# Performance work log

Hardware: AMD Instinct MI355X
Metric: run time of the kernel (lower is better)

## Reference

```python
import jax, jax.numpy as jnp
import numpy as np

NHEADS = 8
HEAD_DIM = 64  # odim // nheads = 512 // 8


def setup_inputs() -> dict:
    key = jax.random.key(0)
    ks = jax.random.split(key, 5)
    B, S, D = 2, 4096, 512
    scale = 1.0 / np.sqrt(D)
    return {
        "m_feats": jax.random.normal(ks[0], (B, S, D), dtype=jnp.float32),
        "Wc": jax.random.normal(ks[1], (2 * D, D), dtype=jnp.float32) * scale,
        "bc": jax.random.normal(ks[2], (2 * D,), dtype=jnp.float32) * 0.01,
        "Wv": jax.random.normal(ks[3], (D, D), dtype=jnp.float32) * scale,
        "bv": jax.random.normal(ks[4], (D,), dtype=jnp.float32) * 0.01,
    }


def reference(m_feats, Wc, bc, Wv, bv):
    # eval mode: dropout(p=0.5) is identity
    B, S, D = m_feats.shape
    H, Dh = NHEADS, HEAD_DIM
    m_k = m_feats @ Wv.T + bv                    # [B,S,D]
    m_trans = m_feats @ Wc.T + bc                # [B,S,2D]
    m_q, m_v = m_trans[..., :D], m_trans[..., D:]
    # torch.split into contiguous per-head chunks == reshape to [B,S,H,Dh]
    k = m_k.reshape(B, S, H, Dh)
    q = m_q.reshape(B, S, H, Dh)
    v = m_v.reshape(B, S, H, Dh)
    # scores[b,h,i,j] = k_i . q_j / sqrt(Dh); softmax over j (the q axis)
    scores = jnp.einsum("bihd,bjhd->bhij", k, q) / np.sqrt(Dh).astype(np.float32)
    w = jax.nn.softmax(scores, axis=-1)          # [B,H,S,S]
    r = jnp.einsum("bhij,bjhd->bihd", w, v).reshape(B, S, D)
    return m_feats + r
```

## Files before the change

kernel.cpp:

```cpp
#include <hip/hip_runtime.h>

#define MTOT 8192

typedef __attribute__((ext_vector_type(8))) short bf16x8;
typedef __attribute__((ext_vector_type(4))) float f32x4;

#if __has_builtin(__builtin_amdgcn_exp2f)
#define EXP2F __builtin_amdgcn_exp2f
#else
#define EXP2F exp2f
#endif

#define SC 0.18033688011112042f
#define LDP 72
#define CTS 136

static __device__ __forceinline__ unsigned short tb(float f) {
  union { float f; unsigned int i; } x;
  x.f = f;
  return (unsigned short)(x.i >> 16);
}
static __device__ __forceinline__ unsigned int pkt(float a, float b) {
  union { float f; unsigned int i; } xa, xb;
  xa.f = a; xb.f = b;
  return (xa.i >> 16) | (xb.i & 0xFFFF0000u);
}
static __device__ __forceinline__ bf16x8 ld8f32_bf16(const float* __restrict__ p) {
  f32x4 lo = *(const f32x4*)p;
  f32x4 hi = *(const f32x4*)(p + 4);
  union { unsigned int u[4]; bf16x8 v; } r;
  r.u[0] = pkt(lo[0], lo[1]);
  r.u[1] = pkt(lo[2], lo[3]);
  r.u[2] = pkt(hi[0], hi[1]);
  r.u[3] = pkt(hi[2], hi[3]);
  return r.v;
}

static __device__ __forceinline__ void stage16(const unsigned short* g,
                                               unsigned short* l, int lane) {
#if __has_builtin(__builtin_amdgcn_global_load_lds)
  __builtin_amdgcn_global_load_lds(
      (const __attribute__((address_space(1))) void*)g,
      (__attribute__((address_space(3))) void*)l, 16, 0, 0);
#else
  *(uint4*)(l + lane * 8) = *(const uint4*)g;
#endif
}

__global__ __launch_bounds__(256) void convert_bf16(
    const float* __restrict__ mf,
    const float* __restrict__ Wc,
    const float* __restrict__ Wv,
    unsigned short* __restrict__ dst)
{
  const size_t NA = (size_t)MTOT * 512;
  const size_t NW = (size_t)1536 * 512;
  const size_t total = (NA + NW) / 8;
  for (size_t u = (size_t)blockIdx.x * blockDim.x + threadIdx.x; u < total;
       u += (size_t)gridDim.x * blockDim.x) {
    const size_t el = u * 8;
    const float* src;
    if (el < NA) {
      src = mf + el;
    } else {
      const size_t e2 = el - NA;
      src = (e2 < (size_t)1024 * 512) ? (Wc + e2) : (Wv + (e2 - (size_t)1024 * 512));
    }
    f32x4 lo = *(const f32x4*)src;
    f32x4 hi = *(const f32x4*)(src + 4);
    uint4 pk;
    pk.x = pkt(lo[0], lo[1]); pk.y = pkt(lo[2], lo[3]);
    pk.z = pkt(hi[0], hi[1]); pk.w = pkt(hi[2], hi[3]);
    *(uint4*)(dst + el) = pk;
  }
}

__global__ __launch_bounds__(256) void gemm_fast(
    const unsigned short* __restrict__ Abf,
    const unsigned short* __restrict__ Wbf,
    const float* __restrict__ bc,
    const float* __restrict__ bv,
    unsigned short* __restrict__ ws)
{
  const int cpx = (int)gridDim.x >> 3;
  const int bid = ((int)blockIdx.x & 7) * cpx + ((int)blockIdx.x >> 3);
  const int tn = bid % 12, tm = bid / 12;
  const int w = threadIdx.x >> 6, lane = threadIdx.x & 63;
  const int n = lane & 15, q = lane >> 4;

  __shared__ alignas(16) unsigned short smem[2 * 128 * LDP];
  unsigned short* As = smem;
  unsigned short* Bs = smem + 128 * 64;

  f32x4 acc[4][4] = {};
  const int rowA0 = tm * 128, colB0 = tn * 128;
  const int lr = lane >> 3;
  const int lc = (lane & 7) * 8;
  const unsigned short* gA = Abf + (size_t)(rowA0 + w * 32 + lr) * 512 + lc;
  const unsigned short* gB = Wbf + (size_t)(colB0 + w * 32 + lr) * 512 + lc;

  for (int kc = 0; kc < 512; kc += 64) {
#pragma unroll
    for (int rr = 0; rr < 4; ++rr) {
      stage16(gA + (size_t)rr * 8 * 512 + kc, As + (w * 32 + rr * 8) * 64, lane);
      stage16(gB + (size_t)rr * 8 * 512 + kc, Bs + (w * 32 + rr * 8) * 64, lane);
    }
    __syncthreads();
#pragma unroll
    for (int ks = 0; ks < 2; ++ks) {
      bf16x8 a[4], b[4];
#pragma unroll
      for (int si = 0; si < 4; ++si)
        a[si] = *(const bf16x8*)(&As[((w >> 1) * 64 + si * 16 + n) * 64 + ks * 32 + q * 8]);
#pragma unroll
      for (int sj = 0; sj < 4; ++sj)
        b[sj] = *(const bf16x8*)(&Bs[((w & 1) * 64 + sj * 16 + n) * 64 + ks * 32 + q * 8]);
#pragma unroll
      for (int si = 0; si < 4; ++si)
#pragma unroll
        for (int sj = 0; sj < 4; ++sj)
          acc[si][sj] = __builtin_amdgcn_mfma_f32_16x16x32_bf16(a[si], b[sj], acc[si][sj], 0, 0, 0);
    }
    __syncthreads();
  }

  unsigned short* Ct = smem;
  const bool isV = (tn >= 4 && tn < 8);
  const int rl0 = (w >> 1) * 64, cl0 = (w & 1) * 64;

  if (!isV) {
    const bool isK = (tn >= 8);
#pragma unroll
    for (int sj = 0; sj < 4; ++sj) {
      const int c = colB0 + sj * 16 + n;
      const float bias = isK ? bv[c - 1024] : bc[c];
#pragma unroll
      for (int si = 0; si < 4; ++si)
#pragma unroll
        for (int r = 0; r < 4; ++r) {
          float v = acc[si][sj][r] + bias;
          if (isK) v *= SC;
          Ct[(rl0 + si * 16 + q * 4 + r) * CTS + cl0 + sj * 16 + n] = tb(v);
        }
    }
  } else {
#pragma unroll
    for (int sj = 0; sj < 4; ++sj) {
      const float bias = bc[colB0 + sj * 16 + n];
#pragma unroll
      for (int si = 0; si < 4; ++si) {
        uint2 pk;
        pk.x = pkt(acc[si][sj][0] + bias, acc[si][sj][1] + bias);
        pk.y = pkt(acc[si][sj][2] + bias, acc[si][sj][3] + bias);
        *(uint2*)(&Ct[(cl0 + sj * 16 + n) * CTS + rl0 + si * 16 + q * 4]) = pk;
      }
    }
  }
  __syncthreads();

  const int rk = threadIdx.x & 7, rr2 = threadIdx.x >> 3;
#pragma unroll
  for (int rp = 0; rp < 4; ++rp) {
    const int row = rp * 32 + rr2;
#pragma unroll
    for (int ch = 0; ch < 2; ++ch) {
      const int col = ch * 64 + rk * 8;
      bf16x8 v = *(const bf16x8*)(&Ct[row * CTS + col]);
      if (!isV) {
        const int srow = rowA0 + row;
        const int bb = srow >> 12, ss = srow & 4095;
        const int cg = colB0 + col;
        const int cl = (cg >= 1024) ? (cg - 1024) : cg;
        const int hh = cl >> 6, dh0 = cl & 63;
        unsigned short* base = (cg >= 1024) ? (ws + (size_t)2 * MTOT * 512) : ws;
        *(bf16x8*)(base + ((size_t)((bb * 8 + hh) * 4096 + ss)) * 64 + dh0) = v;
      } else {
        const int cv = (tn - 4) * 128 + row;
        const int hh = cv >> 6, dh0 = cv & 63;
        const int sg = rowA0 + col;
        const int bb = sg >> 12, ss = sg & 4095;
        *(bf16x8*)(ws + (size_t)MTOT * 512 +
                   ((size_t)((bb * 8 + hh) * 64 + dh0)) * 4096 + ss) = v;
      }
    }
  }
}

__global__ __launch_bounds__(256) void gemm_qvk(
    const float* __restrict__ mf,
    const float* __restrict__ Wc,
    const float* __restrict__ bc,
    const float* __restrict__ Wv,
    const float* __restrict__ bv,
    unsigned short* __restrict__ ws,
    int nct)
{
  const int cpx = (int)gridDim.x >> 3;
  const int bid = ((int)blockIdx.x & 7) * cpx + ((int)blockIdx.x >> 3);
  const int tn = bid % nct, tm = bid / nct;
  const int w = threadIdx.x >> 6, lane = threadIdx.x & 63;
  const int n = lane & 15, q = lane >> 4;

  __shared__ alignas(16) unsigned short smem[2 * 128 * LDP];
  unsigned short* As = smem;
  unsigned short* Bs = smem + 128 * LDP;

  f32x4 acc[4][4] = {};
  const int rowA0 = tm * 128, colB0 = tn * 128;
  const int sr = threadIdx.x >> 4;
  const int sc = (threadIdx.x & 15) * 4;

  for (int kc = 0; kc < 512; kc += 64) {
    __syncthreads();
#pragma unroll
    for (int rr = 0; rr < 8; ++rr) {
      const int row = rr * 16 + sr;
      f32x4 av = *(const f32x4*)(mf + (size_t)(rowA0 + row) * 512 + kc + sc);
      uint2 ap; ap.x = pkt(av[0], av[1]); ap.y = pkt(av[2], av[3]);
      *(uint2*)(&As[row * LDP + sc]) = ap;
      const int c = colB0 + row;
      const float* bsrc = (c < 1024) ? (Wc + (size_t)c * 512)
                                     : (Wv + (size_t)(c - 1024) * 512);
      f32x4 bvx = *(const f32x4*)(bsrc + kc + sc);
      uint2 bp; bp.x = pkt(bvx[0], bvx[1]); bp.y = pkt(bvx[2], bvx[3]);
      *(uint2*)(&Bs[row * LDP + sc]) = bp;
    }
    __syncthreads();
#pragma unroll
    for (int ks = 0; ks < 2; ++ks) {
      bf16x8 a[4], b[4];
#pragma unroll
      for (int si = 0; si < 4; ++si)
        a[si] = *(const bf16x8*)(&As[((w >> 1) * 64 + si * 16 + n) * LDP + ks * 32 + q * 8]);
#pragma unroll
      for (int sj = 0; sj < 4; ++sj)
        b[sj] = *(const bf16x8*)(&Bs[((w & 1) * 64 + sj * 16 + n) * LDP + ks * 32 + q * 8]);
#pragma unroll
      for (int si = 0; si < 4; ++si)
#pragma unroll
        for (int sj = 0; sj < 4; ++sj)
          acc[si][sj] = __builtin_amdgcn_mfma_f32_16x16x32_bf16(a[si], b[sj], acc[si][sj], 0, 0, 0);
    }
  }

  __syncthreads();
  unsigned short* Ct = smem;
  const bool isV = (tn >= 4 && tn < 8);
  const int rl0 = (w >> 1) * 64, cl0 = (w & 1) * 64;

  if (!isV) {
    const bool isK = (tn >= 8);
#pragma unroll
    for (int sj = 0; sj < 4; ++sj) {
      const int c = colB0 + sj * 16 + n;
      const float bias = isK ? bv[c - 1024] : bc[c];
#pragma unroll
      for (int si = 0; si < 4; ++si)
#pragma unroll
        for (int r = 0; r < 4; ++r) {
          float v = acc[si][sj][r] + bias;
          if (isK) v *= SC;
          Ct[(rl0 + si * 16 + q * 4 + r) * CTS + cl0 + sj * 16 + n] = tb(v);
        }
    }
  } else {
#pragma unroll
    for (int sj = 0; sj < 4; ++sj) {
      const float bias = bc[colB0 + sj * 16 + n];
#pragma unroll
      for (int si = 0; si < 4; ++si) {
        uint2 pk;
        pk.x = pkt(acc[si][sj][0] + bias, acc[si][sj][1] + bias);
        pk.y = pkt(acc[si][sj][2] + bias, acc[si][sj][3] + bias);
        *(uint2*)(&Ct[(cl0 + sj * 16 + n) * CTS + rl0 + si * 16 + q * 4]) = pk;
      }
    }
  }
  __syncthreads();

  const int rk = threadIdx.x & 7, rr2 = threadIdx.x >> 3;
#pragma unroll
  for (int rp = 0; rp < 4; ++rp) {
    const int row = rp * 32 + rr2;
#pragma unroll
    for (int ch = 0; ch < 2; ++ch) {
      const int col = ch * 64 + rk * 8;
      bf16x8 v = *(const bf16x8*)(&Ct[row * CTS + col]);
      if (!isV) {
        const int srow = rowA0 + row;
        const int bb = srow >> 12, ss = srow & 4095;
        const int cg = colB0 + col;
        const int cl = (cg >= 1024) ? (cg - 1024) : cg;
        const int hh = cl >> 6, dh0 = cl & 63;
        unsigned short* base = (cg >= 1024) ? (ws + (size_t)2 * MTOT * 512) : ws;
        *(bf16x8*)(base + ((size_t)((bb * 8 + hh) * 4096 + ss)) * 64 + dh0) = v;
      } else {
        const int cv = (tn - 4) * 128 + row;
        const int hh = cv >> 6, dh0 = cv & 63;
        const int sg = rowA0 + col;
        const int bb = sg >> 12, ss = sg & 4095;
        *(bf16x8*)(ws + (size_t)MTOT * 512 +
                   ((size_t)((bb * 8 + hh) * 64 + dh0)) * 4096 + ss) = v;
      }
    }
  }
}

template <bool KWS>
__global__ __launch_bounds__(128, 2) void attn_kernel(
    const unsigned short* __restrict__ qvws,
    const float* __restrict__ mf,
    const float* __restrict__ Wv,
    const float* __restrict__ bv,
    float* __restrict__ out)
{
  const int bid = blockIdx.x;
  const int bh = ((bid & 7) << 1) | ((bid >> 3) & 1);
  const int ib = bid >> 4;
  const int b_ = bh >> 3, h = bh & 7;
  const int w = threadIdx.x >> 6, lane = threadIdx.x & 63;
  const int n = lane & 15, q = lane >> 4;
  const int i0 = ib * 64;

  __shared__ alignas(16) unsigned short PK[2][64 * LDP];
  __shared__ float lbuf[2][64];

  const unsigned short* Qb = qvws + (size_t)(bh * 4096) * 64;
  const unsigned short* Vb = qvws + (size_t)MTOT * 512 + (size_t)(bh * 64) * 4096;

  bf16x8 aK[4][2];
  if (KWS) {
    const unsigned short* Kb = qvws + (size_t)2 * MTOT * 512 + (size_t)(bh * 4096) * 64;
#pragma unroll
    for (int sub = 0; sub < 4; ++sub)
#pragma unroll
      for (int s = 0; s < 2; ++s)
        aK[sub][s] = *(const bf16x8*)(Kb + (size_t)(i0 + sub * 16 + n) * 64 + s * 32 + q * 8);
  } else {
    f32x4 ka[2][4] = {};
    for (int kk = 0; kk < 512; kk += 32) {
      bf16x8 a0 = ld8f32_bf16(mf + (size_t)(b_ * 4096 + i0 + (2 * w + 0) * 16 + n) * 512 + kk + q * 8);
      bf16x8 a1 = ld8f32_bf16(mf + (size_t)(b_ * 4096 + i0 + (2 * w + 1) * 16 + n) * 512 + kk + q * 8);
#pragma unroll
      for (int t = 0; t < 4; ++t) {
        bf16x8 bw = ld8f32_bf16(Wv + (size_t)(h * 64 + t * 16 + n) * 512 + kk + q * 8);
        ka[0][t] = __builtin_amdgcn_mfma_f32_16x16x32_bf16(a0, bw, ka[0][t], 0, 0, 0);
        ka[1][t] = __builtin_amdgcn_mfma_f32_16x16x32_bf16(a1, bw, ka[1][t], 0, 0, 0);
      }
    }
#pragma unroll
    for (int sl = 0; sl < 2; ++sl)
#pragma unroll
      for (int t = 0; t < 4; ++t) {
        const float bias = bv[h * 64 + t * 16 + n];
#pragma unroll
        for (int r = 0; r < 4; ++r)
          PK[0][((2 * w + sl) * 16 + q * 4 + r) * LDP + t * 16 + n] =
              tb((ka[sl][t][r] + bias) * SC);
      }
    __syncthreads();
#pragma unroll
    for (int sub = 0; sub < 4; ++sub)
#pragma unroll
      for (int s = 0; s < 2; ++s)
        aK[sub][s] = *(const bf16x8*)(&PK[0][(sub * 16 + n) * LDP + s * 32 + q * 8]);
    __syncthreads();
  }

  f32x4 o[4][4] = {};
  float lsc[4] = {0.0f, 0.0f, 0.0f, 0.0f};
  unsigned short* Pw = &PK[w][0];
  const int jbase = w * 2048;

  bf16x8 bq[4][2], bvv[4][2];
#pragma unroll
  for (int jt = 0; jt < 4; ++jt)
#pragma unroll
    for (int s = 0; s < 2; ++s)
      bq[jt][s] = *(const bf16x8*)(Qb + (size_t)(jbase + jt * 16 + n) * 64 + s * 32 + q * 8);
#pragma unroll
  for (int t = 0; t < 4; ++t)
#pragma unroll
    for (int s = 0; s < 2; ++s)
      bvv[t][s] = *(const bf16x8*)(Vb + (size_t)(t * 16 + n) * 4096 + jbase + s * 32 + q * 8);

  for (int it = 0; it < 32; ++it) {
    const int j1 = jbase + ((it + 1) & 31) * 64;

    f32x4 c[2][4];
#pragma unroll
    for (int jt = 0; jt < 4; ++jt) {
      f32x4 z = {};
      z = __builtin_amdgcn_mfma_f32_16x16x32_bf16(bq[jt][0], aK[0][0], z, 0, 0, 0);
      z = __builtin_amdgcn_mfma_f32_16x16x32_bf16(bq[jt][1], aK[0][1], z, 0, 0, 0);
      c[0][jt] = z;
    }

#pragma unroll
    for (int sub = 0; sub < 4; ++sub) {
      const int cur = sub & 1, nxt = cur ^ 1;
      if (sub < 3) {
#pragma unroll
        for (int jt = 0; jt < 4; ++jt) {
          f32x4 z = {};
          z = __builtin_amdgcn_mfma_f32_16x16x32_bf16(bq[jt][0], aK[sub + 1][0], z, 0, 0, 0);
          z = __builtin_amdgcn_mfma_f32_16x16x32_bf16(bq[jt][1], aK[sub + 1][1], z, 0, 0, 0);
          c[nxt][jt] = z;
        }
      }
      if (sub == 2) {
#pragma unroll
        for (int jt = 0; jt < 4; ++jt)
#pragma unroll
          for (int s = 0; s < 2; ++s)
            bq[jt][s] = *(const bf16x8*)(Qb + (size_t)(j1 + jt * 16 + n) * 64 + s * 32 + q * 8);
      }

#pragma unroll
      for (int jt = 0; jt < 4; ++jt) {
        float e0 = EXP2F(c[cur][jt][0]), e1 = EXP2F(c[cur][jt][1]);
        float e2 = EXP2F(c[cur][jt][2]), e3 = EXP2F(c[cur][jt][3]);
        lsc[sub] += (e0 + e1) + (e2 + e3);
        uint2 pk;
        pk.x = pkt(e0, e1);
        pk.y = pkt(e2, e3);
        *(uint2*)(Pw + (sub * 16 + n) * LDP + jt * 16 + q * 4) = pk;
      }

      asm volatile("s_waitcnt lgkmcnt(0)" ::: "memory");

#pragma unroll
      for (int s = 0; s < 2; ++s) {
        bf16x8 pa = *(const bf16x8*)(Pw + (sub * 16 + n) * LDP + s * 32 + q * 8);
#pragma unroll
        for (int t = 0; t < 4; ++t)
          o[sub][t] = __builtin_amdgcn_mfma_f32_16x16x32_bf16(pa, bvv[t][s], o[sub][t], 0, 0, 0);
      }
    }

#pragma unroll
    for (int t = 0; t < 4; ++t)
#pragma unroll
      for (int s = 0; s < 2; ++s)
        bvv[t][s] = *(const bf16x8*)(Vb + (size_t)(t * 16 + n) * 4096 + j1 + s * 32 + q * 8);
  }

  float lw[4];
#pragma unroll
  for (int sub = 0; sub < 4; ++sub) {
    float v = lsc[sub];
    v += __shfl_xor(v, 16, 64);
    v += __shfl_xor(v, 32, 64);
    lw[sub] = v;
  }

  __syncthreads();
  float* mO = (float*)&PK[0][0];
  const int ebase = (w == 0) ? 0 : 32;
  const int rbase = (w == 0) ? 32 : 0;
  const int esub0 = (w == 0) ? 2 : 0;
  const int ksub0 = (w == 0) ? 0 : 2;
#pragma unroll
  for (int sl = 0; sl < 2; ++sl) {
    const int sub = esub0 + sl;
#pragma unroll
    for (int t = 0; t < 4; ++t)
#pragma unroll
      for (int r = 0; r < 4; ++r)
        mO[(ebase + sl * 16 + q * 4 + r) * 68 + t * 16 + n] = o[sub][t][r];
  }
  if (lane < 16) {
#pragma unroll
    for (int sub = 0; sub < 4; ++sub)
      lbuf[w][sub * 16 + lane] = lw[sub];
  }
  __syncthreads();
#pragma unroll
  for (int sl = 0; sl < 2; ++sl) {
    const int sub = ksub0 + sl;
    float li[4];
#pragma unroll
    for (int r = 0; r < 4; ++r) {
      const int il = sub * 16 + q * 4 + r;
      li[r] = 1.0f / (lbuf[0][il] + lbuf[1][il]);
    }
#pragma unroll
    for (int t = 0; t < 4; ++t) {
#pragma unroll
      for (int r = 0; r < 4; ++r) {
        const int i = i0 + sub * 16 + q * 4 + r;
        const int dh = t * 16 + n;
        const size_t idx = (size_t)(b_ * 4096 + i) * 512 + h * 64 + dh;
        out[idx] = (o[sub][t][r] + mO[(rbase + sl * 16 + q * 4 + r) * 68 + t * 16 + n]) * li[r]
                   + mf[idx];
      }
    }
  }
}

extern "C" void kernel_launch(void* const* d_in, const int* in_sizes, int n_in,
                              void* d_out, int out_size, void* d_ws, size_t ws_size,
                              hipStream_t stream) {
  const float* mf = (const float*)d_in[0];
  const float* Wc = (const float*)d_in[1];
  const float* bc = (const float*)d_in[2];
  const float* Wv = (const float*)d_in[3];
  const float* bv = (const float*)d_in[4];
  float* out = (float*)d_out;
  unsigned short* ws = (unsigned short*)d_ws;

  const size_t elQ = (size_t)MTOT * 512;
  const bool kws = ws_size >= (size_t)3 * elQ * 2;

  if (kws) {
    unsigned short* Abf = (unsigned short*)out;
    unsigned short* Wbf = Abf + (size_t)MTOT * 512;
    convert_bf16<<<2048, 256, 0, stream>>>(mf, Wc, Wv, Abf);
    gemm_fast<<<768, 256, 0, stream>>>(Abf, Wbf, bc, bv, ws);
    attn_kernel<true><<<1024, 128, 0, stream>>>(ws, mf, Wv, bv, out);
  } else {
    gemm_qvk<<<64 * 8, 256, 0, stream>>>(mf, Wc, bc, Wv, bv, ws, 8);
    attn_kernel<false><<<1024, 128, 0, stream>>>(ws, mf, Wv, bv, out);
  }
}
```

Before: 237.1 us.

## Use 128x64 tiles with XOR-swizzled LDS in projection GEMM

The bf16 projection GEMM moves from 128x128 to 128x64 output tiles, which doubles the grid to 1536 blocks and shrinks the shared-memory footprint. LDS staging now uses an XOR swizzle on 16-byte chunks to avoid bank conflicts on unpadded rows. The epilogue is reworked for the narrower tile, using a separate stride for the Q/K staging buffer. The goal is better occupancy and wave balance across CUs and fewer LDS conflicts, at the cost of less A-tile reuse per block.

```diff
diff --git a/kernel.cpp b/kernel.cpp
--- a/kernel.cpp
+++ b/kernel.cpp
@@ -14,6 +14,7 @@
 #define SC 0.18033688011112042f
 #define LDP 72
 #define CTS 136
+#define CTQ 72
 
 static __device__ __forceinline__ unsigned short tb(float f) {
   union { float f; unsigned int i; } x;
@@ -84,26 +85,152 @@
 {
   const int cpx = (int)gridDim.x >> 3;
   const int bid = ((int)blockIdx.x & 7) * cpx + ((int)blockIdx.x >> 3);
-  const int tn = bid % 12, tm = bid / 12;
+  const int tn = bid % 24, tm = bid / 24;
   const int w = threadIdx.x >> 6, lane = threadIdx.x & 63;
   const int n = lane & 15, q = lane >> 4;
 
+  __shared__ alignas(16) unsigned short smem[128 * 64 + 64 * 64];
+  unsigned short* As = smem;
+  unsigned short* Bs = smem + 128 * 64;
+
+  f32x4 acc[4][2] = {};
+  const int rowA0 = tm * 128, colB0 = tn * 64;
+  const int lrow = lane >> 3;
+  const int sw = ((lane & 7) ^ lrow) * 8;
+  const unsigned short* gA = Abf + (size_t)(rowA0 + w * 32 + lrow) * 512 + sw;
+  const unsigned short* gB = Wbf + (size_t)(colB0 + w * 16 + lrow) * 512 + sw;
+
+  for (int kc = 0; kc < 512; kc += 64) {
+#pragma unroll
+    for (int rr = 0; rr < 4; ++rr)
+      stage16(gA + (size_t)rr * 8 * 512 + kc, As + (w * 32 + rr * 8) * 64, lane);
+#pragma unroll
+    for (int rr = 0; rr < 2; ++rr)
+      stage16(gB + (size_t)rr * 8 * 512 + kc, Bs + (w * 16 + rr * 8) * 64, lane);
+    __syncthreads();
+#pragma unroll
+    for (int ks = 0; ks < 2; ++ks) {
+      const int ch = ((ks * 4 + q) ^ (n & 7)) * 8;
+      bf16x8 a[4], b[2];
+#pragma unroll
+      for (int si = 0; si < 4; ++si)
+        a[si] = *(const bf16x8*)(&As[((w >> 1) * 64 + si * 16 + n) * 64 + ch]);
+#pragma unroll
+      for (int sj = 0; sj < 2; ++sj)
+        b[sj] = *(const bf16x8*)(&Bs[((w & 1) * 32 + sj * 16 + n) * 64 + ch]);
+#pragma unroll
+      for (int si = 0; si < 4; ++si)
+#pragma unroll
+        for (int sj = 0; sj < 2; ++sj)
+          acc[si][sj] = __builtin_amdgcn_mfma_f32_16x16x32_bf16(a[si], b[sj], acc[si][sj], 0, 0, 0);
+    }
+    __syncthreads();
+  }
+
+  unsigned short* Ct = smem;
+  const bool isV = (tn >= 8 && tn < 16);
+  const int rl0 = (w >> 1) * 64, cl0 = (w & 1) * 32;
+
+  if (!isV) {
+    const bool isK = (tn >= 16);
+#pragma unroll
+    for (int sj = 0; sj < 2; ++sj) {
+      const int c = colB0 + cl0 + sj * 16 + n;
+      const float bias = isK ? bv[c - 1024] : bc[c];
+#pragma unroll
+      for (int si = 0; si < 4; ++si)
+#pragma unroll
+        for (int r = 0; r < 4; ++r) {
+          float v = acc[si][sj][r] + bias;
+          if (isK) v *= SC;
+          Ct[(rl0 + si * 16 + q * 4 + r) * CTQ + cl0 + sj * 16 + n] = tb(v);
+        }
+    }
+  } else {
+#pragma unroll
+    for (int sj = 0; sj < 2; ++sj) {
+      const float bias = bc[colB0 + cl0 + sj * 16 + n];
+#pragma unroll
+      for (int si = 0; si < 4; ++si) {
+        uint2 pk;
+        pk.x = pkt(acc[si][sj][0] + bias, acc[si][sj][1] + bias);
+        pk.y = pkt(acc[si][sj][2] + bias, acc[si][sj][3] + bias);
+        *(uint2*)(&Ct[(cl0 + sj * 16 + n) * CTS + rl0 + si * 16 + q * 4]) = pk;
+      }
+    }
+  }
+  __syncthreads();
+
+  if (!isV) {
+    const int rk = threadIdx.x & 7, rr2 = threadIdx.x >> 3;
+#pragma unroll
+    for (int rp = 0; rp < 4; ++rp) {
+      const int row = rp * 32 + rr2;
+      const int col = rk * 8;
+      bf16x8 v = *(const bf16x8*)(&Ct[row * CTQ + col]);
+      const int srow = rowA0 + row;
+      const int bb = srow >> 12, ss = srow & 4095;
+      const int cg = colB0 + col;
+      const int cl = (cg >= 1024) ? (cg - 1024) : cg;
+      const int hh = cl >> 6, dh0 = cl & 63;
+      unsigned short* base = (cg >= 1024) ? (ws + (size_t)2 * MTOT * 512) : ws;
+      *(bf16x8*)(base + ((size_t)((bb * 8 + hh) * 4096 + ss)) * 64 + dh0) = v;
+    }
+  } else {
+    const int rk = threadIdx.x & 15, rr2 = threadIdx.x >> 4;
+#pragma unroll
+    for (int rp = 0; rp < 4; ++rp) {
+      const int row = rp * 16 + rr2;
+      const int col = rk * 8;
+      bf16x8 v = *(const bf16x8*)(&Ct[row * CTS + col]);
+      const int cv = (tn - 8) * 64 + row;
+      const int hh = cv >> 6, dh0 = cv & 63;
+      const int sg = rowA0 + col;
+      const int bb = sg >> 12, ss = sg & 4095;
+      *(bf16x8*)(ws + (size_t)MTOT * 512 +
+                 ((size_t)((bb * 8 + hh) * 64 + dh0)) * 4096 + ss) = v;
+    }
+  }
+}
+
+__global__ __launch_bounds__(256) void gemm_qvk(
+    const float* __restrict__ mf,
+    const float* __restrict__ Wc,
+    const float* __restrict__ bc,
+    const float* __restrict__ Wv,
+    const float* __restrict__ bv,
+    unsigned short* __restrict__ ws,
+    int nct)
+{
+  const int cpx = (int)gridDim.x >> 3;
+  const int bid = ((int)blockIdx.x & 7) * cpx + ((int)blockIdx.x >> 3);
+  const int tn = bid % nct, tm = bid / nct;
+  const int w = threadIdx.x >> 6, lane = threadIdx.x & 63;
+  const int n = lane & 15, q = lane >> 4;
+
   __shared__ alignas(16) unsigned short smem[2 * 128 * LDP];
   unsigned short* As = smem;
-  unsigned short* Bs = smem + 128 * 64;
+  unsigned short* Bs = smem + 128 * LDP;
 
   f32x4 acc[4][4] = {};
   const int rowA0 = tm * 128, colB0 = tn * 128;
-  const int lr = lane >> 3;
-  const int lc = (lane & 7) * 8;
-  const unsigned short* gA = Abf + (size_t)(rowA0 + w * 32 + lr) * 512 + lc;
-  const unsigned short* gB = Wbf + (size_t)(colB0 + w * 32 + lr) * 512 + lc;
+  const int sr = threadIdx.x >> 4;
+  const int sc = (threadIdx.x & 15) * 4;
 
   for (int kc = 0; kc < 512; kc += 64) {
-#pragma unroll
-    for (int rr = 0; rr < 4; ++rr) {
-      stage16(gA + (size_t)rr * 8 * 512 + kc, As + (w * 32 + rr * 8) * 64, lane);
-      stage16(gB + (size_t)rr * 8 * 512 + kc, Bs + (w * 32 + rr * 8) * 64, lane);
+    __syncthreads();
+#pragma unroll
+    for (int rr = 0; rr < 8; ++rr) {
+      const int row = rr * 16 + sr;
+      f32x4 av = *(const f32x4*)(mf + (size_t)(rowA0 + row) * 512 + kc + sc);
+      uint2 ap; ap.x = pkt(av[0], av[1]); ap.y = pkt(av[2], av[3]);
+      *(uint2*)(&As[row * LDP + sc]) = ap;
+      const int c = colB0 + row;
+      const float* bsrc = (c < 1024) ? (Wc + (size_t)c * 512)
+                                     : (Wv + (size_t)(c - 1024) * 512);
+      f32x4 bvx = *(const f32x4*)(bsrc + kc + sc);
+      uint2 bp; bp.x = pkt(bvx[0], bvx[1]); bp.y = pkt(bvx[2], bvx[3]);
+      *(uint2*)(&Bs[row * LDP + sc]) = bp;
     }
     __syncthreads();
 #pragma unroll
@@ -111,19 +238,19 @@
       bf16x8 a[4], b[4];
 #pragma unroll
       for (int si = 0; si < 4; ++si)
-        a[si] = *(const bf16x8*)(&As[((w >> 1) * 64 + si * 16 + n) * 64 + ks * 32 + q * 8]);
+        a[si] = *(const bf16x8*)(&As[((w >> 1) * 64 + si * 16 + n) * LDP + ks * 32 + q * 8]);
 #pragma unroll
       for (int sj = 0; sj < 4; ++sj)
-        b[sj] = *(const bf16x8*)(&Bs[((w & 1) * 64 + sj * 16 + n) * 64 + ks * 32 + q * 8]);
+        b[sj] = *(const bf16x8*)(&Bs[((w & 1) * 64 + sj * 16 + n) * LDP + ks * 32 + q * 8]);
 #pragma unroll
       for (int si = 0; si < 4; ++si)
 #pragma unroll
         for (int sj = 0; sj < 4; ++sj)
           acc[si][sj] = __builtin_amdgcn_mfma_f32_16x16x32_bf16(a[si], b[sj], acc[si][sj], 0, 0, 0);
     }
-    __syncthreads();
-  }
-
+  }
+
+  __syncthreads();
   unsigned short* Ct = smem;
   const bool isV = (tn >= 4 && tn < 8);
   const int rl0 = (w >> 1) * 64, cl0 = (w & 1) * 64;
@@ -186,126 +313,6 @@
   }
 }
 
-__global__ __launch_bounds__(256) void gemm_qvk(
-    const float* __restrict__ mf,
-    const float* __restrict__ Wc,
-    const float* __restrict__ bc,
-    const float* __restrict__ Wv,
-    const float* __restrict__ bv,
-    unsigned short* __restrict__ ws,
-    int nct)
-{
-  const int cpx = (int)gridDim.x >> 3;
-  const int bid = ((int)blockIdx.x & 7) * cpx + ((int)blockIdx.x >> 3);
-  const int tn = bid % nct, tm = bid / nct;
-  const int w = threadIdx.x >> 6, lane = threadIdx.x & 63;
-  const int n = lane & 15, q = lane >> 4;
-
-  __shared__ alignas(16) unsigned short smem[2 * 128 * LDP];
-  unsigned short* As = smem;
-  unsigned short* Bs = smem + 128 * LDP;
-
-  f32x4 acc[4][4] = {};
-  const int rowA0 = tm * 128, colB0 = tn * 128;
-  const int sr = threadIdx.x >> 4;
-  const int sc = (threadIdx.x & 15) * 4;
-
-  for (int kc = 0; kc < 512; kc += 64) {
-    __syncthreads();
-#pragma unroll
-    for (int rr = 0; rr < 8; ++rr) {
-      const int row = rr * 16 + sr;
-      f32x4 av = *(const f32x4*)(mf + (size_t)(rowA0 + row) * 512 + kc + sc);
-      uint2 ap; ap.x = pkt(av[0], av[1]); ap.y = pkt(av[2], av[3]);
-      *(uint2*)(&As[row * LDP + sc]) = ap;
-      const int c = colB0 + row;
-      const float* bsrc = (c < 1024) ? (Wc + (size_t)c * 512)
-                                     : (Wv + (size_t)(c - 1024) * 512);
-      f32x4 bvx = *(const f32x4*)(bsrc + kc + sc);
-      uint2 bp; bp.x = pkt(bvx[0], bvx[1]); bp.y = pkt(bvx[2], bvx[3]);
-      *(uint2*)(&Bs[row * LDP + sc]) = bp;
-    }
-    __syncthreads();
-#pragma unroll
-    for (int ks = 0; ks < 2; ++ks) {
-      bf16x8 a[4], b[4];
-#pragma unroll
-      for (int si = 0; si < 4; ++si)
-        a[si] = *(const bf16x8*)(&As[((w >> 1) * 64 + si * 16 + n) * LDP + ks * 32 + q * 8]);
-#pragma unroll
-      for (int sj = 0; sj < 4; ++sj)
-        b[sj] = *(const bf16x8*)(&Bs[((w & 1) * 64 + sj * 16 + n) * LDP + ks * 32 + q * 8]);
-#pragma unroll
-      for (int si = 0; si < 4; ++si)
-#pragma unroll
-        for (int sj = 0; sj < 4; ++sj)
-          acc[si][sj] = __builtin_amdgcn_mfma_f32_16x16x32_bf16(a[si], b[sj], acc[si][sj], 0, 0, 0);
-    }
-  }
-
-  __syncthreads();
-  unsigned short* Ct = smem;
-  const bool isV = (tn >= 4 && tn < 8);
-  const int rl0 = (w >> 1) * 64, cl0 = (w & 1) * 64;
-
-  if (!isV) {
-    const bool isK = (tn >= 8);
-#pragma unroll
-    for (int sj = 0; sj < 4; ++sj) {
-      const int c = colB0 + sj * 16 + n;
-      const float bias = isK ? bv[c - 1024] : bc[c];
-#pragma unroll
-      for (int si = 0; si < 4; ++si)
-#pragma unroll
-        for (int r = 0; r < 4; ++r) {
-          float v = acc[si][sj][r] + bias;
-          if (isK) v *= SC;
-          Ct[(rl0 + si * 16 + q * 4 + r) * CTS + cl0 + sj * 16 + n] = tb(v);
-        }
-    }
-  } else {
-#pragma unroll
-    for (int sj = 0; sj < 4; ++sj) {
-      const float bias = bc[colB0 + sj * 16 + n];
-#pragma unroll
-      for (int si = 0; si < 4; ++si) {
-        uint2 pk;
-        pk.x = pkt(acc[si][sj][0] + bias, acc[si][sj][1] + bias);
-        pk.y = pkt(acc[si][sj][2] + bias, acc[si][sj][3] + bias);
-        *(uint2*)(&Ct[(cl0 + sj * 16 + n) * CTS + rl0 + si * 16 + q * 4]) = pk;
-      }
-    }
-  }
-  __syncthreads();
-
-  const int rk = threadIdx.x & 7, rr2 = threadIdx.x >> 3;
-#pragma unroll
-  for (int rp = 0; rp < 4; ++rp) {
-    const int row = rp * 32 + rr2;
-#pragma unroll
-    for (int ch = 0; ch < 2; ++ch) {
-      const int col = ch * 64 + rk * 8;
-      bf16x8 v = *(const bf16x8*)(&Ct[row * CTS + col]);
-      if (!isV) {
-        const int srow = rowA0 + row;
-        const int bb = srow >> 12, ss = srow & 4095;
-        const int cg = colB0 + col;
-        const int cl = (cg >= 1024) ? (cg - 1024) : cg;
-        const int hh = cl >> 6, dh0 = cl & 63;
-        unsigned short* base = (cg >= 1024) ? (ws + (size_t)2 * MTOT * 512) : ws;
-        *(bf16x8*)(base + ((size_t)((bb * 8 + hh) * 4096 + ss)) * 64 + dh0) = v;
-      } else {
-        const int cv = (tn - 4) * 128 + row;
-        const int hh = cv >> 6, dh0 = cv & 63;
-        const int sg = rowA0 + col;
-        const int bb = sg >> 12, ss = sg & 4095;
-        *(bf16x8*)(ws + (size_t)MTOT * 512 +
-                   ((size_t)((bb * 8 + hh) * 64 + dh0)) * 4096 + ss) = v;
-      }
-    }
-  }
-}
-
 template <bool KWS>
 __global__ __launch_bounds__(128, 2) void attn_kernel(
     const unsigned short* __restrict__ qvws,
@@ -516,7 +523,7 @@
     unsigned short* Abf = (unsigned short*)out;
     unsigned short* Wbf = Abf + (size_t)MTOT * 512;
     convert_bf16<<<2048, 256, 0, stream>>>(mf, Wc, Wv, Abf);
-    gemm_fast<<<768, 256, 0, stream>>>(Abf, Wbf, bc, bv, ws);
+    gemm_fast<<<1536, 256, 0, stream>>>(Abf, Wbf, bc, bv, ws);
     attn_kernel<true><<<1024, 128, 0, stream>>>(ws, mf, Wv, bv, out);
   } else {
     gemm_qvk<<<64 * 8, 256, 0, stream>>>(mf, Wc, bc, Wv, bv, ws, 8);
```

Measured after the change: 231.2 us. -2.5%, faster.
